# Performance work log

Hardware: AMD Instinct MI355X
Metric: run time of the kernel (lower is better)

## Reference

```python
import jax, jax.numpy as jnp
import numpy as np

N = 50000      # nodes
E = 1600000    # edges (avg degree 32)
D_IN = 128
HID = 64


def setup_inputs() -> dict:
    key = jax.random.key(0)
    ks = jax.random.split(key, 7)
    x = jax.random.normal(ks[0], (N, D_IN), dtype=jnp.float32)
    ei = jax.random.randint(ks[1], (2, E), 0, N, dtype=jnp.int32)
    ew = jax.random.uniform(ks[2], (E,), dtype=jnp.float32)
    # GCNConv linear weights (glorot-ish scale); lin has no bias, conv bias added post-aggregation
    W1 = jax.random.normal(ks[3], (HID, D_IN), dtype=jnp.float32) * (1.0 / np.sqrt(D_IN))
    b1 = jnp.zeros((HID,), dtype=jnp.float32)
    W2 = jax.random.normal(ks[4], (HID, HID), dtype=jnp.float32) * (1.0 / np.sqrt(HID))
    b2 = jnp.zeros((HID,), dtype=jnp.float32)
    return {"x": x, "ei": ei, "ew": ew, "W1": W1, "b1": b1, "W2": W2, "b2": b2}


def _gcn_conv(x, src, dst, ew_all, W, b, n_nodes):
    """PyG GCNConv: gcn_norm (self-loops already appended) + x@W.T, gather-scale-scatter, +b."""
    deg = jax.ops.segment_sum(ew_all, dst, num_segments=n_nodes)  # dst-side weighted degree
    dinv = jnp.where(deg > 0, jax.lax.rsqrt(deg), 0.0)            # deg^{-1/2}, inf->0
    norm = dinv[src] * ew_all * dinv[dst]                          # [E+N]
    h = x @ W.T                                                    # [N, hid]
    msg = h[src] * norm[:, None]                                   # gather + scale
    out = jax.ops.segment_sum(msg, dst, num_segments=n_nodes)     # scatter-add
    return out + b


def reference(x, ei, ew, W1, b1, W2, b2):
    n_nodes = x.shape[0]
    # add self loops once (fill value 1.0), shared by both conv layers
    loop = jnp.arange(n_nodes, dtype=ei.dtype)
    src = jnp.concatenate([ei[0], loop])
    dst = jnp.concatenate([ei[1], loop])
    ew_all = jnp.concatenate([ew, jnp.ones((n_nodes,), dtype=ew.dtype)])

    h1 = jax.nn.relu(_gcn_conv(x, src, dst, ew_all, W1, b1, n_nodes))
    # dropout is identity in eval mode
    h2 = _gcn_conv(h1, src, dst, ew_all, W2, b2, n_nodes)
    return h2 + h1
```

## Files before the change

kernel.cpp:

```cpp
#include <hip/hip_runtime.h>

#define HID 64
#define DIN 128
#define NBLK 512
#define CSH 14
#define CAP (1 << CSH)
#define PAD 68

typedef unsigned long long ull;
typedef unsigned short u16;

static __device__ __forceinline__ u16 f2bf(float f) {
  unsigned u = __float_as_uint(f);
  unsigned lsb = (u >> 16) & 1u;
  u += 0x7fffu + lsb;
  return (u16)(u >> 16);
}


template <int K, bool XT_PRELOADED>
__device__ __forceinline__ void gemm_tile(const float* __restrict__ X,
                                          const float* __restrict__ W,
                                          u16* __restrict__ out,
                                          float* XT, float* WL,
                                          int n0, int n_nodes, int tid) {
  const int tx = tid & 15;
  const int ty = tid >> 4;
  float acc[2][4] = {{0.f}};

  for (int ph = 0; ph < K / 64; ++ph) {
    const int d0 = ph * 64;
    __syncthreads();
    if (!XT_PRELOADED) {
#pragma unroll
      for (int k = 0; k < 2; ++k) {
        int f = tid + k * 512;
        int r = f >> 4, q = f & 15;
        int n = n0 + r;
        float4 xv = (n < n_nodes)
          ? *reinterpret_cast<const float4*>(&X[(size_t)n * K + d0 + 4 * q])
          : make_float4(0.f, 0.f, 0.f, 0.f);
        *reinterpret_cast<float4*>(&XT[r * PAD + 4 * q]) = xv;
      }
    }
#pragma unroll
    for (int k = 0; k < 2; ++k) {
      int gq = tid + k * 512;
      int qd = gq >> 6, j = gq & 63;
      float4 wv = *reinterpret_cast<const float4*>(&W[(size_t)j * K + d0 + 4 * qd]);
      WL[(4 * qd + 0) * PAD + j] = wv.x;
      WL[(4 * qd + 1) * PAD + j] = wv.y;
      WL[(4 * qd + 2) * PAD + j] = wv.z;
      WL[(4 * qd + 3) * PAD + j] = wv.w;
    }
    __syncthreads();
#pragma unroll 4
    for (int dd = 0; dd < 64; dd += 4) {
      float4 ws[4];
#pragma unroll
      for (int dk = 0; dk < 4; ++dk)
        ws[dk] = *reinterpret_cast<const float4*>(&WL[(dd + dk) * PAD + 4 * tx]);
      float4 x0 = *reinterpret_cast<const float4*>(&XT[ty * PAD + dd]);
      float4 x1 = *reinterpret_cast<const float4*>(&XT[(ty + 32) * PAD + dd]);
      float xm0[4] = {x0.x, x0.y, x0.z, x0.w};
      float xm1[4] = {x1.x, x1.y, x1.z, x1.w};
#pragma unroll
      for (int dk = 0; dk < 4; ++dk) {
        acc[0][0] = fmaf(xm0[dk], ws[dk].x, acc[0][0]);
        acc[0][1] = fmaf(xm0[dk], ws[dk].y, acc[0][1]);
        acc[0][2] = fmaf(xm0[dk], ws[dk].z, acc[0][2]);
        acc[0][3] = fmaf(xm0[dk], ws[dk].w, acc[0][3]);
        acc[1][0] = fmaf(xm1[dk], ws[dk].x, acc[1][0]);
        acc[1][1] = fmaf(xm1[dk], ws[dk].y, acc[1][1]);
        acc[1][2] = fmaf(xm1[dk], ws[dk].z, acc[1][2]);
        acc[1][3] = fmaf(xm1[dk], ws[dk].w, acc[1][3]);
      }
    }
  }

#pragma unroll
  for (int mi = 0; mi < 2; ++mi) {
    int n = n0 + mi * 32 + ty;
    if (n < n_nodes) {
      ushort4 o = make_ushort4(f2bf(acc[mi][0]), f2bf(acc[mi][1]),
                               f2bf(acc[mi][2]), f2bf(acc[mi][3]));
      *reinterpret_cast<ushort4*>(&out[(size_t)n * HID + 4 * tx]) = o;
    }
  }
}


__global__ __launch_bounds__(512) void k_build_gemm(const int* __restrict__ src,
                                                    const int* __restrict__ dst,
                                                    const float* __restrict__ ew,
                                                    int* __restrict__ cursor,
                                                    int2* __restrict__ bufA,
                                                    int E, int chunk,
                                                    const float* __restrict__ x,
                                                    const float* __restrict__ W1,
                                                    u16* __restrict__ h,
                                                    int n_nodes) {
  __shared__ float S[2 * 64 * PAD];
  int b = blockIdx.x, tid = threadIdx.x;
  if (b >= NBLK) {
    gemm_tile<DIN, false>(x, W1, h, S, S + 64 * PAD, (b - NBLK) * 64, n_nodes, tid);
    return;
  }
  int* hst = (int*)S;
  int* cur = (int*)S + 256;
  if (tid < 256) hst[tid] = 0;
  __syncthreads();
  int e0 = b * chunk, e1 = min(E, e0 + chunk);
  int nfull = (e1 - e0) & ~3;
  int rtail = (e1 - e0) - nfull;
  for (int e = e0 + 4 * tid; e < e0 + nfull; e += 4 * 512) {
    int4 d4 = *reinterpret_cast<const int4*>(&dst[e]);
    atomicAdd(&hst[d4.x >> 8], 1);
    atomicAdd(&hst[d4.y >> 8], 1);
    atomicAdd(&hst[d4.z >> 8], 1);
    atomicAdd(&hst[d4.w >> 8], 1);
  }
  if (tid < rtail) atomicAdd(&hst[dst[e0 + nfull + tid] >> 8], 1);
  __syncthreads();
  if (tid < 256) {
    int c = hst[tid];
    int ofs = (c > 0) ? atomicAdd(&cursor[tid], c) : 0;
    cur[tid] = (tid << CSH) + ofs;
  }
  __syncthreads();
  for (int e = e0 + 4 * tid; e < e0 + nfull; e += 4 * 512) {
    int4 s4 = *reinterpret_cast<const int4*>(&src[e]);
    int4 d4 = *reinterpret_cast<const int4*>(&dst[e]);
    float4 w4 = *reinterpret_cast<const float4*>(&ew[e]);
    int p0 = atomicAdd(&cur[d4.x >> 8], 1);
    bufA[p0] = make_int2(__float_as_int(w4.x), (int)(((unsigned)s4.x << 16) | (unsigned)d4.x));
    int p1 = atomicAdd(&cur[d4.y >> 8], 1);
    bufA[p1] = make_int2(__float_as_int(w4.y), (int)(((unsigned)s4.y << 16) | (unsigned)d4.y));
    int p2 = atomicAdd(&cur[d4.z >> 8], 1);
    bufA[p2] = make_int2(__float_as_int(w4.z), (int)(((unsigned)s4.z << 16) | (unsigned)d4.z));
    int p3 = atomicAdd(&cur[d4.w >> 8], 1);
    bufA[p3] = make_int2(__float_as_int(w4.w), (int)(((unsigned)s4.w << 16) | (unsigned)d4.w));
  }
  if (tid < rtail) {
    int e = e0 + nfull + tid;
    int s = src[e], d = dst[e];
    int p = atomicAdd(&cur[d >> 8], 1);
    bufA[p] = make_int2(__float_as_int(ew[e]), (int)(((unsigned)s << 16) | (unsigned)d));
  }
}


__global__ __launch_bounds__(1024) void k_passB(const int2* __restrict__ bufA,
                                                const int* __restrict__ cursor,
                                                int2* __restrict__ bufB,
                                                int* __restrict__ offs,
                                                int* __restrict__ cnt,
                                                float* __restrict__ dinv,
                                                int NBC, int N) {
  int bin = blockIdx.x, tid = threadIdx.x;
  __shared__ int h2[256];
  __shared__ int cur[256];
  __shared__ float dg[256];
  int bbase = bin << CSH;
  int m = cursor[bin];
  if (tid < 256) { h2[tid] = 0; dg[tid] = 0.f; }
  __syncthreads();
  int2 rloc[16];
#pragma unroll
  for (int k = 0; k < 16; ++k) {
    int i = tid + k * 1024;
    if (i < m) {
      rloc[k] = bufA[bbase + i];
      atomicAdd(&h2[(unsigned)rloc[k].y & 255u], 1);
    }
  }
  __syncthreads();
  int own = (tid < 256) ? h2[tid] : 0;
  for (int o = 1; o < 256; o <<= 1) {
    int u = 0;
    if (tid < 256 && tid >= o) u = h2[tid - o];
    __syncthreads();
    if (tid < 256) h2[tid] += u;
    __syncthreads();
  }
  int nd = (bin << 8) + tid;
  if (tid < 256) {
    int excl = h2[tid] - own;
    cur[tid] = excl;
    if (nd < N) { offs[nd] = bbase + excl; cnt[nd] = own; }
  }
  __syncthreads();
#pragma unroll
  for (int k = 0; k < 16; ++k) {
    int i = tid + k * 1024;
    if (i < m) {
      int2 r = rloc[k];
      unsigned sd = (unsigned)r.y;
      int dl = (int)(sd & 255u);
      int p = atomicAdd(&cur[dl], 1);
      bufB[bbase + p] = make_int2(r.x, (int)(sd >> 16));
      atomicAdd(&dg[dl], __int_as_float(r.x));
    }
  }
  __syncthreads();
  if (tid < 256 && nd < N) dinv[nd] = rsqrtf(1.0f + dg[tid]);
}


__device__ __forceinline__ void bfma8(const uint4& v, float w, float* a) {
  a[0] = fmaf(__uint_as_float(v.x << 16), w, a[0]);
  a[1] = fmaf(__uint_as_float(v.x & 0xffff0000u), w, a[1]);
  a[2] = fmaf(__uint_as_float(v.y << 16), w, a[2]);
  a[3] = fmaf(__uint_as_float(v.y & 0xffff0000u), w, a[3]);
  a[4] = fmaf(__uint_as_float(v.z << 16), w, a[4]);
  a[5] = fmaf(__uint_as_float(v.z & 0xffff0000u), w, a[5]);
  a[6] = fmaf(__uint_as_float(v.w << 16), w, a[6]);
  a[7] = fmaf(__uint_as_float(v.w & 0xffff0000u), w, a[7]);
}

__device__ __forceinline__ void agg_node(const u16* __restrict__ h,
                                         const int2* __restrict__ recs,
                                         const float* __restrict__ dinv,
                                         int beg, int end, int node, float di,
                                         int lane, int p8, float* r) {
  float a[8], b[8];
  {
    uint4 v = *reinterpret_cast<const uint4*>(&h[(size_t)node * HID + p8]);
    a[0] = __uint_as_float(v.x << 16) * di;
    a[1] = __uint_as_float(v.x & 0xffff0000u) * di;
    a[2] = __uint_as_float(v.y << 16) * di;
    a[3] = __uint_as_float(v.y & 0xffff0000u) * di;
    a[4] = __uint_as_float(v.z << 16) * di;
    a[5] = __uint_as_float(v.z & 0xffff0000u) * di;
    a[6] = __uint_as_float(v.w << 16) * di;
    a[7] = __uint_as_float(v.w & 0xffff0000u) * di;
#pragma unroll
    for (int j = 0; j < 8; ++j) b[j] = 0.f;
  }

  const int gb = lane & 56;
  int i = beg;
  while (i + 8 <= end) {
    ull rr = *reinterpret_cast<const ull*>(&recs[i + (lane & 7)]);
    float wd = __uint_as_float((unsigned)rr) * dinv[(int)(rr >> 32)];
    rr = (rr & 0xffffffff00000000ull) | (ull)__float_as_uint(wd);
#pragma unroll
    for (int k = 0; k < 8; ++k) {
      ull q = __shfl(rr, gb | k, 64);
      float wk = __uint_as_float((unsigned)q);
      int sk = (int)(q >> 32);
      uint4 vk = *reinterpret_cast<const uint4*>(&h[(size_t)sk * HID + p8]);
      bfma8(vk, wk, (k & 1) ? b : a);
    }
    i += 8;
  }
  if (i + 4 <= end) {
    int2 r0 = recs[i];     int2 r1 = recs[i + 1];
    int2 r2 = recs[i + 2]; int2 r3 = recs[i + 3];
    uint4 v0 = *reinterpret_cast<const uint4*>(&h[(size_t)r0.y * HID + p8]);
    uint4 v1 = *reinterpret_cast<const uint4*>(&h[(size_t)r1.y * HID + p8]);
    uint4 v2 = *reinterpret_cast<const uint4*>(&h[(size_t)r2.y * HID + p8]);
    uint4 v3 = *reinterpret_cast<const uint4*>(&h[(size_t)r3.y * HID + p8]);
    bfma8(v0, __int_as_float(r0.x) * dinv[r0.y], a);
    bfma8(v1, __int_as_float(r1.x) * dinv[r1.y], b);
    bfma8(v2, __int_as_float(r2.x) * dinv[r2.y], a);
    bfma8(v3, __int_as_float(r3.x) * dinv[r3.y], b);
    i += 4;
  }
  if (i + 2 <= end) {
    int2 r0 = recs[i];     int2 r1 = recs[i + 1];
    uint4 v0 = *reinterpret_cast<const uint4*>(&h[(size_t)r0.y * HID + p8]);
    uint4 v1 = *reinterpret_cast<const uint4*>(&h[(size_t)r1.y * HID + p8]);
    bfma8(v0, __int_as_float(r0.x) * dinv[r0.y], a);
    bfma8(v1, __int_as_float(r1.x) * dinv[r1.y], b);
    i += 2;
  }
  if (i < end) {
    int2 r0 = recs[i];
    uint4 v0 = *reinterpret_cast<const uint4*>(&h[(size_t)r0.y * HID + p8]);
    bfma8(v0, __int_as_float(r0.x) * dinv[r0.y], a);
  }
#pragma unroll
  for (int j = 0; j < 8; ++j) r[j] = (a[j] + b[j]) * di;
}


__global__ __launch_bounds__(512) void k_agg_gemm(const u16* __restrict__ h,
                                                  const int2* __restrict__ recs,
                                                  const int* __restrict__ offs,
                                                  const int* __restrict__ cnt,
                                                  const float* __restrict__ dinv,
                                                  const float* __restrict__ bias,
                                                  const float* __restrict__ W2,
                                                  float* __restrict__ h1,
                                                  u16* __restrict__ h2,
                                                  int n_nodes) {
  __shared__ float S[2 * 64 * PAD];
  float* XT = S;
  float* WL = S + 64 * PAD;
  int tid = threadIdx.x;
  int lane = tid & 63;
  int p8 = (lane & 7) * 8;
  int nl = (tid >> 6) * 8 + (lane >> 3);
  int node = blockIdx.x * 64 + nl;
  if (node < n_nodes) {
    float di = dinv[node];
    float r[8];
    agg_node(h, recs, dinv, offs[node], offs[node] + cnt[node], node, di,
             lane, p8, r);
    float4 bb0 = *reinterpret_cast<const float4*>(&bias[p8]);
    float4 bb1 = *reinterpret_cast<const float4*>(&bias[p8 + 4]);
    r[0] += bb0.x; r[1] += bb0.y; r[2] += bb0.z; r[3] += bb0.w;
    r[4] += bb1.x; r[5] += bb1.y; r[6] += bb1.z; r[7] += bb1.w;
#pragma unroll
    for (int j = 0; j < 8; ++j) r[j] = fmaxf(r[j], 0.f);
    float4 lo = make_float4(r[0], r[1], r[2], r[3]);
    float4 hi = make_float4(r[4], r[5], r[6], r[7]);
    *reinterpret_cast<float4*>(&h1[(size_t)node * HID + p8]) = lo;
    *reinterpret_cast<float4*>(&h1[(size_t)node * HID + p8 + 4]) = hi;
    *reinterpret_cast<float4*>(&XT[nl * PAD + p8]) = lo;
    *reinterpret_cast<float4*>(&XT[nl * PAD + p8 + 4]) = hi;
  }
  gemm_tile<HID, true>(nullptr, W2, h2, XT, WL, blockIdx.x * 64, n_nodes, tid);
}


__global__ __launch_bounds__(256) void k_agg2(const u16* __restrict__ h,
                                              const int2* __restrict__ recs,
                                              const int* __restrict__ offs,
                                              const int* __restrict__ cnt,
                                              const float* __restrict__ dinv,
                                              const float* __restrict__ bias,
                                              const float* __restrict__ resid,
                                              float* __restrict__ out, int n_nodes) {
  int tid = threadIdx.x;
  int lane = tid & 63;
  int p8 = (lane & 7) * 8;
  int node = (blockIdx.x * 4 + (tid >> 6)) * 8 + (lane >> 3);
  if (node >= n_nodes) return;
  float di = dinv[node];
  float r[8];
  agg_node(h, recs, dinv, offs[node], offs[node] + cnt[node], node, di,
           lane, p8, r);
  float4 bb0 = *reinterpret_cast<const float4*>(&bias[p8]);
  float4 bb1 = *reinterpret_cast<const float4*>(&bias[p8 + 4]);
  float4 rs0 = *reinterpret_cast<const float4*>(&resid[(size_t)node * HID + p8]);
  float4 rs1 = *reinterpret_cast<const float4*>(&resid[(size_t)node * HID + p8 + 4]);
  r[0] += bb0.x + rs0.x; r[1] += bb0.y + rs0.y;
  r[2] += bb0.z + rs0.z; r[3] += bb0.w + rs0.w;
  r[4] += bb1.x + rs1.x; r[5] += bb1.y + rs1.y;
  r[6] += bb1.z + rs1.z; r[7] += bb1.w + rs1.w;
  *reinterpret_cast<float4*>(&out[(size_t)node * HID + p8]) =
      make_float4(r[0], r[1], r[2], r[3]);
  *reinterpret_cast<float4*>(&out[(size_t)node * HID + p8 + 4]) =
      make_float4(r[4], r[5], r[6], r[7]);
}


extern "C" void kernel_launch(void* const* d_in, const int* in_sizes, int n_in,
                              void* d_out, int out_size, void* d_ws, size_t ws_size,
                              hipStream_t stream) {
  const float* x  = (const float*)d_in[0];
  const int*   ei = (const int*)d_in[1];
  const float* ew = (const float*)d_in[2];
  const float* W1 = (const float*)d_in[3];
  const float* b1 = (const float*)d_in[4];
  const float* W2 = (const float*)d_in[5];
  const float* b2 = (const float*)d_in[6];
  float* out = (float*)d_out;

  const int N = in_sizes[0] / DIN;
  const int E = in_sizes[2];
  const int* src = ei;
  const int* dst = ei + E;

  const int NBC = (N + 255) >> 8;
  const int chunk = (((E + NBLK - 1) / NBLK) + 3) & ~3;
  const int nslab = NBC << CSH;

  char* p = (char*)d_ws;
  auto carve = [&](size_t bytes) {
    char* r = p;
    p += (bytes + 255) & ~(size_t)255;
    return r;
  };
  int*   cursor = (int*)carve(256 * 4);
  int*   offs   = (int*)carve((size_t)N * 4);
  int*   cnt    = (int*)carve((size_t)N * 4);
  float* dinv   = (float*)carve((size_t)N * 4);
  int2*  bufA   = (int2*)carve((size_t)nslab * 8);
  int2*  bufB   = (int2*)carve((size_t)nslab * 8);
  u16*   h      = (u16*)carve((size_t)N * HID * 2);
  u16*   h2     = (u16*)carve((size_t)N * HID * 2);
  float* h1     = (float*)carve((size_t)N * HID * 4);

  int gblk = (N + 63) / 64;
  int ablk = (N + 31) / 32;

  hipMemsetAsync(cursor, 0, 256 * 4, stream);
  k_build_gemm<<<NBLK + gblk, 512, 0, stream>>>(src, dst, ew, cursor, bufA, E, chunk,
                                                x, W1, h, N);
  k_passB<<<NBC, 1024, 0, stream>>>(bufA, cursor, bufB, offs, cnt, dinv, NBC, N);
  k_agg_gemm<<<gblk, 512, 0, stream>>>(h, bufB, offs, cnt, dinv, b1, W2, h1, h2, N);
  k_agg2<<<ablk, 256, 0, stream>>>(h2, bufB, offs, cnt, dinv, b2, h1, out, N);
}
```

Baseline: 215.9 us.

## Prefetch next edge-record batch in aggregation and shrink agg_gemm blocks to 256 threads

The aggregation inner loop now loads the next batch of 8 edge records and their dinv values before processing the current batch, a software-pipelining step meant to hide the dependent record-to-dinv load latency. Separately, the fused aggregation+GEMM kernel is retiled to 32 nodes per 256-thread block, with gemm_tile templated on thread count. Smaller blocks reduce LDS per block and let more blocks fit per CU, which should help hide latency and balance load, at the cost of more W2 loads into shared memory per node.

```diff
diff --git a/kernel.cpp b/kernel.cpp
--- a/kernel.cpp
+++ b/kernel.cpp
@@ -18,12 +18,13 @@
 }
 
 
-template <int K, bool XT_PRELOADED>
+template <int K, int NT, bool XT_PRELOADED>
 __device__ __forceinline__ void gemm_tile(const float* __restrict__ X,
                                           const float* __restrict__ W,
                                           u16* __restrict__ out,
                                           float* XT, float* WL,
                                           int n0, int n_nodes, int tid) {
+  constexpr int ROWS = NT / 8;
   const int tx = tid & 15;
   const int ty = tid >> 4;
   float acc[2][4] = {{0.f}};
@@ -34,7 +35,7 @@
     if (!XT_PRELOADED) {
 #pragma unroll
       for (int k = 0; k < 2; ++k) {
-        int f = tid + k * 512;
+        int f = tid + k * NT;
         int r = f >> 4, q = f & 15;
         int n = n0 + r;
         float4 xv = (n < n_nodes)
@@ -44,8 +45,8 @@
       }
     }
 #pragma unroll
-    for (int k = 0; k < 2; ++k) {
-      int gq = tid + k * 512;
+    for (int k = 0; k < 1024 / NT; ++k) {
+      int gq = tid + k * NT;
       int qd = gq >> 6, j = gq & 63;
       float4 wv = *reinterpret_cast<const float4*>(&W[(size_t)j * K + d0 + 4 * qd]);
       WL[(4 * qd + 0) * PAD + j] = wv.x;
@@ -61,7 +62,7 @@
       for (int dk = 0; dk < 4; ++dk)
         ws[dk] = *reinterpret_cast<const float4*>(&WL[(dd + dk) * PAD + 4 * tx]);
       float4 x0 = *reinterpret_cast<const float4*>(&XT[ty * PAD + dd]);
-      float4 x1 = *reinterpret_cast<const float4*>(&XT[(ty + 32) * PAD + dd]);
+      float4 x1 = *reinterpret_cast<const float4*>(&XT[(ty + ROWS / 2) * PAD + dd]);
       float xm0[4] = {x0.x, x0.y, x0.z, x0.w};
       float xm1[4] = {x1.x, x1.y, x1.z, x1.w};
 #pragma unroll
@@ -80,7 +81,7 @@
 
 #pragma unroll
   for (int mi = 0; mi < 2; ++mi) {
-    int n = n0 + mi * 32 + ty;
+    int n = n0 + mi * (ROWS / 2) + ty;
     if (n < n_nodes) {
       ushort4 o = make_ushort4(f2bf(acc[mi][0]), f2bf(acc[mi][1]),
                                f2bf(acc[mi][2]), f2bf(acc[mi][3]));
@@ -103,7 +104,7 @@
   __shared__ float S[2 * 64 * PAD];
   int b = blockIdx.x, tid = threadIdx.x;
   if (b >= NBLK) {
-    gemm_tile<DIN, false>(x, W1, h, S, S + 64 * PAD, (b - NBLK) * 64, n_nodes, tid);
+    gemm_tile<DIN, 512, false>(x, W1, h, S, S + 64 * PAD, (b - NBLK) * 64, n_nodes, tid);
     return;
   }
   int* hst = (int*)S;
@@ -239,20 +240,32 @@
   }
 
   const int gb = lane & 56;
+  const int l7 = lane & 7;
   int i = beg;
-  while (i + 8 <= end) {
-    ull rr = *reinterpret_cast<const ull*>(&recs[i + (lane & 7)]);
-    float wd = __uint_as_float((unsigned)rr) * dinv[(int)(rr >> 32)];
-    rr = (rr & 0xffffffff00000000ull) | (ull)__float_as_uint(wd);
-#pragma unroll
-    for (int k = 0; k < 8; ++k) {
-      ull q = __shfl(rr, gb | k, 64);
-      float wk = __uint_as_float((unsigned)q);
-      int sk = (int)(q >> 32);
-      uint4 vk = *reinterpret_cast<const uint4*>(&h[(size_t)sk * HID + p8]);
-      bfma8(vk, wk, (k & 1) ? b : a);
-    }
-    i += 8;
+  if (i + 8 <= end) {
+    ull rr = *reinterpret_cast<const ull*>(&recs[i + l7]);
+    float dv = dinv[(int)(rr >> 32)];
+    for (;;) {
+      float wd = __uint_as_float((unsigned)rr) * dv;
+      ull ru = (rr & 0xffffffff00000000ull) | (ull)__float_as_uint(wd);
+      bool more = (i + 16 <= end);
+      ull rr_n = 0; float dv_n = 0.f;
+      if (more) {
+        rr_n = *reinterpret_cast<const ull*>(&recs[i + 8 + l7]);
+        dv_n = dinv[(int)(rr_n >> 32)];
+      }
+#pragma unroll
+      for (int k = 0; k < 8; ++k) {
+        ull q = __shfl(ru, gb | k, 64);
+        float wk = __uint_as_float((unsigned)q);
+        int sk = (int)(q >> 32);
+        uint4 vk = *reinterpret_cast<const uint4*>(&h[(size_t)sk * HID + p8]);
+        bfma8(vk, wk, (k & 1) ? b : a);
+      }
+      i += 8;
+      if (!more) break;
+      rr = rr_n; dv = dv_n;
+    }
   }
   if (i + 4 <= end) {
     int2 r0 = recs[i];     int2 r1 = recs[i + 1];
@@ -285,7 +298,7 @@
 }
 
 
-__global__ __launch_bounds__(512) void k_agg_gemm(const u16* __restrict__ h,
+__global__ __launch_bounds__(256) void k_agg_gemm(const u16* __restrict__ h,
                                                   const int2* __restrict__ recs,
                                                   const int* __restrict__ offs,
                                                   const int* __restrict__ cnt,
@@ -295,14 +308,14 @@
                                                   float* __restrict__ h1,
                                                   u16* __restrict__ h2,
                                                   int n_nodes) {
-  __shared__ float S[2 * 64 * PAD];
+  __shared__ float S[(32 + 64) * PAD];
   float* XT = S;
-  float* WL = S + 64 * PAD;
+  float* WL = S + 32 * PAD;
   int tid = threadIdx.x;
   int lane = tid & 63;
   int p8 = (lane & 7) * 8;
   int nl = (tid >> 6) * 8 + (lane >> 3);
-  int node = blockIdx.x * 64 + nl;
+  int node = blockIdx.x * 32 + nl;
   if (node < n_nodes) {
     float di = dinv[node];
     float r[8];
@@ -321,7 +334,7 @@
     *reinterpret_cast<float4*>(&XT[nl * PAD + p8]) = lo;
     *reinterpret_cast<float4*>(&XT[nl * PAD + p8 + 4]) = hi;
   }
-  gemm_tile<HID, true>(nullptr, W2, h2, XT, WL, blockIdx.x * 64, n_nodes, tid);
+  gemm_tile<HID, 256, true>(nullptr, W2, h2, XT, WL, blockIdx.x * 32, n_nodes, tid);
 }
 
 
@@ -394,13 +407,14 @@
   u16*   h2     = (u16*)carve((size_t)N * HID * 2);
   float* h1     = (float*)carve((size_t)N * HID * 4);
 
-  int gblk = (N + 63) / 64;
-  int ablk = (N + 31) / 32;
+  int gblk  = (N + 63) / 64;
+  int gblk2 = (N + 31) / 32;
+  int ablk  = (N + 31) / 32;
 
   hipMemsetAsync(cursor, 0, 256 * 4, stream);
   k_build_gemm<<<NBLK + gblk, 512, 0, stream>>>(src, dst, ew, cursor, bufA, E, chunk,
                                                 x, W1, h, N);
   k_passB<<<NBC, 1024, 0, stream>>>(bufA, cursor, bufB, offs, cnt, dinv, NBC, N);
-  k_agg_gemm<<<gblk, 512, 0, stream>>>(h, bufB, offs, cnt, dinv, b1, W2, h1, h2, N);
+  k_agg_gemm<<<gblk2, 256, 0, stream>>>(h, bufB, offs, cnt, dinv, b1, W2, h1, h2, N);
   k_agg2<<<ablk, 256, 0, stream>>>(h2, bufB, offs, cnt, dinv, b2, h1, out, N);
 }
```

After: 209.5 us. 1.03x faster.
